# Optimization experiments

Hardware: AMD Instinct MI355X
Metric: run time of the kernel (lower is better)

Reference implementation:

```python
import jax, jax.numpy as jnp
import numpy as np

N_HEAD = 16

def setup_inputs() -> dict:
    key = jax.random.key(0)
    k1, k2 = jax.random.split(key)
    B, T, C = 4, 2048, 1024
    x = jax.random.normal(k1, (B, T, C), dtype=jnp.float32)
    # fused QKV projection weight, stored as [C, 3C] so qkv = x @ w_qkv
    # (equivalent to torch Linear(C, 3C, bias=False) with weight.T)
    w_qkv = jax.random.normal(k2, (C, 3 * C), dtype=jnp.float32) * (1.0 / np.sqrt(C))
    return {"x": x, "w_qkv": w_qkv}

def reference(x, w_qkv):
    B, T, C = x.shape
    H = N_HEAD
    D = C // H
    qkv = x @ w_qkv                                  # [B, T, 3C]
    q, k, v = jnp.split(qkv, 3, axis=2)              # each [B, T, C]
    q = q.reshape(B, T, H, D).transpose(0, 2, 1, 3)  # [B, H, T, D]
    k = k.reshape(B, T, H, D).transpose(0, 2, 1, 3)
    v = v.reshape(B, T, H, D).transpose(0, 2, 1, 3)
    scale = np.float32(1.0 / np.sqrt(D))
    att = jnp.einsum('bhqd,bhkd->bhqk', q, k) * scale   # [B, H, T, T]
    causal = jnp.tril(jnp.ones((T, T), dtype=bool))     # lower-tri = visible
    att = jnp.where(causal, att, -jnp.inf)
    att = jax.nn.softmax(att, axis=-1)
    out = jnp.einsum('bhqk,bhkd->bhqd', att, v)          # [B, H, T, D]
    return out.transpose(0, 2, 1, 3).reshape(B, T, C)
```

## Files before the change

kernel.cpp:

```cpp
#include <hip/hip_runtime.h>


#define B_ 4
#define T_ 2048
#define C_ 1024
#define H_ 16
#define D_ 64
#define QKV1 (B_*H_*T_*D_)

typedef __attribute__((ext_vector_type(4)))  float  f32x4;
typedef __attribute__((ext_vector_type(16))) float  f32x16;
typedef __attribute__((ext_vector_type(8)))  short  bf16x8;
typedef __attribute__((ext_vector_type(4)))  unsigned int u32x4;

__device__ inline unsigned short f2bf(float f) {
  unsigned int u = __builtin_bit_cast(unsigned int, f);
  u += 0x7FFFu + ((u >> 16) & 1u);
  return (unsigned short)(u >> 16);
}

__device__ inline void gload16(const unsigned short* g, unsigned short* l) {
  __builtin_amdgcn_global_load_lds(
      (const __attribute__((address_space(1))) void*)g,
      (__attribute__((address_space(3))) void*)l, 16, 0, 0);
}

__global__ __launch_bounds__(256) void convert_x(const float* __restrict__ x,
                                                 unsigned short* __restrict__ xb) {
  size_t i = ((size_t)blockIdx.x * 256 + threadIdx.x) * 16;
  f32x4 a = *(const f32x4*)(x + i);
  f32x4 b = *(const f32x4*)(x + i + 4);
  f32x4 c = *(const f32x4*)(x + i + 8);
  f32x4 d = *(const f32x4*)(x + i + 12);
  bf16x8 o0, o1;
#pragma unroll
  for (int j = 0; j < 4; j++) {
    o0[j]     = (short)f2bf(a[j]);
    o0[j + 4] = (short)f2bf(b[j]);
    o1[j]     = (short)f2bf(c[j]);
    o1[j + 4] = (short)f2bf(d[j]);
  }
  *(bf16x8*)(xb + i) = o0;
  *(bf16x8*)(xb + i + 8) = o1;
}

__global__ __launch_bounds__(256) void transpose_w(const float* __restrict__ w,
                                                   unsigned short* __restrict__ wt) {
  __shared__ float tile[32][33];
  const int tx = threadIdx.x & 31, ty = threadIdx.x >> 5;
  const int n0 = blockIdx.x * 32, k0 = blockIdx.y * 32;
#pragma unroll
  for (int j = 0; j < 4; j++) {
    int k = ty + j * 8;
    tile[k][tx] = w[(size_t)(k0 + k) * 3072 + n0 + tx];
  }
  __syncthreads();
#pragma unroll
  for (int j = 0; j < 4; j++) {
    int n = ty + j * 8;
    wt[(size_t)(n0 + n) * 1024 + k0 + tx] = f2bf(tile[tx][n]);
  }
}

__global__ __launch_bounds__(256) void qkv_gemm(const unsigned short* __restrict__ xb,
                                                const unsigned short* __restrict__ wt,
                                                unsigned short* __restrict__ qkv) {
  __shared__ unsigned short Al[128 * 64];
  __shared__ unsigned short Bl[128 * 64];
  const int tid = threadIdx.x;
  const int lane = tid & 63, wid = tid >> 6;
  const int l15 = lane & 15, g = lane >> 4;
  const int m0 = blockIdx.y * 128, n0 = blockIdx.x * 128;
  const int wm = (wid >> 1) * 64, wn = (wid & 1) * 64;

  f32x4 acc[4][4] = {};

  const int srow[4] = { (0 * 256 + tid) >> 3, (1 * 256 + tid) >> 3,
                        (2 * 256 + tid) >> 3, (3 * 256 + tid) >> 3 };
  int scol[4];
#pragma unroll
  for (int sw = 0; sw < 4; sw++) {
    int s = sw * 256 + tid;
    scol[sw] = (s & 7) ^ (srow[sw] & 7);
  }

  for (int k0 = 0; k0 < 1024; k0 += 64) {
    __syncthreads();
#pragma unroll
    for (int sw = 0; sw < 4; sw++) {
      unsigned short* ldsA = &Al[(sw * 256 + wid * 64) * 8];
      unsigned short* ldsB = &Bl[(sw * 256 + wid * 64) * 8];
      gload16(xb + (size_t)(m0 + srow[sw]) * 1024 + k0 + scol[sw] * 8, ldsA);
      gload16(wt + (size_t)(n0 + srow[sw]) * 1024 + k0 + scol[sw] * 8, ldsB);
    }
    __syncthreads();

#pragma unroll
    for (int ks = 0; ks < 2; ks++) {
      bf16x8 af[4], bfr[4];
#pragma unroll
      for (int mt = 0; mt < 4; mt++) {
        int row = wm + mt * 16 + l15;
        int c = (ks * 4 + g) ^ (row & 7);
        af[mt] = *(const bf16x8*)&Al[(row * 8 + c) * 8];
      }
#pragma unroll
      for (int nt = 0; nt < 4; nt++) {
        int row = wn + nt * 16 + l15;
        int c = (ks * 4 + g) ^ (row & 7);
        bfr[nt] = *(const bf16x8*)&Bl[(row * 8 + c) * 8];
      }
#pragma unroll
      for (int mt = 0; mt < 4; mt++)
#pragma unroll
        for (int nt = 0; nt < 4; nt++)
          acc[mt][nt] = __builtin_amdgcn_mfma_f32_16x16x32_bf16(af[mt], bfr[nt], acc[mt][nt], 0, 0, 0);
    }
  }

  const int r0 = g * 4, cc = l15;
#pragma unroll
  for (int mt = 0; mt < 4; mt++)
#pragma unroll
    for (int nt = 0; nt < 4; nt++)
#pragma unroll
      for (int r = 0; r < 4; r++) {
        int m = m0 + wm + mt * 16 + r0 + r;
        int n = n0 + wn + nt * 16 + cc;
        int b = m >> 11, t = m & 2047;
        int which = n >> 10, c = n & 1023;
        int h = c >> 6, d = c & 63;
        qkv[(size_t)which * QKV1 + ((size_t)((b * H_ + h) * T_ + t)) * D_ + d] =
            f2bf(acc[mt][nt][r]);
      }
}

__global__ __launch_bounds__(256) void attn(const unsigned short* __restrict__ qkv,
                                            float* __restrict__ out) {
  __shared__ unsigned short Kl[64][72];
  __shared__ unsigned short Vl[64][72];
  __shared__ float RSl[4][32];
  const int tid = threadIdx.x, lane = tid & 63, wq = tid >> 6;
  const int l31 = lane & 31, hi = lane >> 5;
  const int bh = blockIdx.y, xp = blockIdx.x;
  const int qta = xp, qtb = 31 - xp;
  const int ntiles = qtb + 1;
  const int member = wq >> 1;
  const int half = wq & 1;
  const int qt = member ? qta : qtb;
  const int q0 = qt * 64 + half * 32;
  const size_t base = (size_t)bh * (T_ * D_);
  const unsigned short* qp = qkv + base;
  const unsigned short* kp = qkv + (size_t)QKV1 + base;
  const unsigned short* vp = qkv + 2 * (size_t)QKV1 + base;

  bf16x8 qf[4];
#pragma unroll
  for (int c = 0; c < 4; c++) {
    bf16x8 v = *(const bf16x8*)(qp + (size_t)(q0 + l31) * 64 + c * 16 + hi * 8);
#pragma unroll
    for (int j = 0; j < 8; j++) {
      unsigned int u = (unsigned int)(unsigned short)v[j] << 16;
      float f = __builtin_bit_cast(float, u) * 0.125f;
      v[j] = (short)f2bf(f);
    }
    qf[c] = v;
  }

  f32x16 o0 = {}, o1 = {};
  float rs = 0.f;

  bf16x8 kreg0, kreg1, vreg0, vreg1;
  const int krow = tid >> 3, kch = tid & 7;
  const int vpr = tid >> 3, vdch = tid & 7;
#define LOADKV(IT)                                                             \
  do {                                                                         \
    size_t k0_ = (size_t)(IT) * 64;                                            \
    kreg0 = *(const bf16x8*)(kp + (k0_ + krow) * 64 + kch * 8);                \
    kreg1 = *(const bf16x8*)(kp + (k0_ + 32 + krow) * 64 + kch * 8);           \
    vreg0 = *(const bf16x8*)(vp + (k0_ + 2 * vpr) * 64 + vdch * 8);            \
    vreg1 = *(const bf16x8*)(vp + (k0_ + 2 * vpr + 1) * 64 + vdch * 8);        \
  } while (0)

  LOADKV(0);
  for (int it = 0; it < ntiles; ++it) {
    __syncthreads();
    *(bf16x8*)&Kl[krow][kch * 8] = kreg0;
    *(bf16x8*)&Kl[32 + krow][kch * 8] = kreg1;
#pragma unroll
    for (int j = 0; j < 8; j++) {
      int d = vdch * 8 + j;
      unsigned int pk = ((unsigned int)(unsigned short)vreg1[j] << 16) |
                        (unsigned int)(unsigned short)vreg0[j];
      *(unsigned int*)&Vl[d][(2 * vpr) ^ ((d >> 3) << 3)] = pk;
    }
    if (it + 1 < ntiles) LOADKV(it + 1);
    __syncthreads();

    if (it <= qt) {
      unsigned int pk_[16];
#pragma unroll
      for (int kt = 0; kt < 2; kt++) {
        f32x16 s = {};
        __builtin_amdgcn_s_setprio(1);
#pragma unroll
        for (int c = 0; c < 4; c++) {
          bf16x8 kf = *(const bf16x8*)&Kl[kt * 32 + l31][c * 16 + hi * 8];
          s = __builtin_amdgcn_mfma_f32_32x32x16_bf16(kf, qf[c], s, 0, 0, 0);
        }
        __builtin_amdgcn_s_setprio(0);
        if (it == qt) {
#pragma unroll
          for (int r = 0; r < 16; r++) {
            int kg = it * 64 + kt * 32 + (r & 3) + 8 * (r >> 2) + 4 * hi;
            if (kg > q0 + l31) s[r] = -1e30f;
          }
        }
        float p[16];
#pragma unroll
        for (int r = 0; r < 16; r++) { p[r] = __expf(s[r]); rs += p[r]; }
#pragma unroll
        for (int t = 0; t < 4; t++) {
          unsigned int plo, phi;
          asm("v_cvt_pk_bf16_f32 %0, %1, %2" : "=v"(plo) : "v"(p[4*t]), "v"(p[4*t+1]));
          asm("v_cvt_pk_bf16_f32 %0, %1, %2" : "=v"(phi) : "v"(p[4*t+2]), "v"(p[4*t+3]));
          pk_[(kt * 4 + t) * 2]     = plo;
          pk_[(kt * 4 + t) * 2 + 1] = phi;
        }
      }

      unsigned int rcv0[4], rcv1[4];
#pragma unroll
      for (int j = 0; j < 4; j++) {
        unsigned int s0 = hi ? pk_[(2 * j) * 2]     : pk_[(2 * j + 1) * 2];
        unsigned int s1 = hi ? pk_[(2 * j) * 2 + 1] : pk_[(2 * j + 1) * 2 + 1];
        rcv0[j] = (unsigned int)__shfl_xor((int)s0, 32);
        rcv1[j] = (unsigned int)__shfl_xor((int)s1, 32);
      }

      __builtin_amdgcn_s_setprio(1);
#pragma unroll
      for (int st = 0; st < 4; st++) {
        unsigned int u0 = hi ? rcv0[st]        : pk_[4 * st];
        unsigned int u1 = hi ? rcv1[st]        : pk_[4 * st + 1];
        unsigned int u2 = hi ? pk_[4 * st + 2] : rcv0[st];
        unsigned int u3 = hi ? pk_[4 * st + 3] : rcv1[st];
        u32x4 pu = {u0, u1, u2, u3};
        bf16x8 paf = __builtin_bit_cast(bf16x8, pu);
        int koff = st * 16 + hi * 8;
        bf16x8 vf0 = *(const bf16x8*)&Vl[l31][koff ^ ((l31 >> 3) << 3)];
        bf16x8 vf1 = *(const bf16x8*)&Vl[32 + l31][koff ^ (((32 + l31) >> 3) << 3)];
        o0 = __builtin_amdgcn_mfma_f32_32x32x16_bf16(paf, vf0, o0, 0, 0, 0);
        o1 = __builtin_amdgcn_mfma_f32_32x32x16_bf16(paf, vf1, o1, 0, 0, 0);
      }
      __builtin_amdgcn_s_setprio(0);
    }
  }

  float rsf = rs + __shfl_xor(rs, 32);
  float inv = 1.0f / rsf;
  if (hi == 0) RSl[wq][l31] = inv;
  asm volatile("s_waitcnt lgkmcnt(0)" ::: "memory");
  const int b = bh >> 4, h = bh & 15;
#pragma unroll
  for (int r = 0; r < 16; r++) {
    int ql = (r & 3) + 8 * (r >> 2) + 4 * hi;
    float iv = RSl[wq][ql];
    int qg = q0 + ql;
    size_t o = ((size_t)(b * T_ + qg)) * C_ + h * 64;
    out[o + l31]      = o0[r] * iv;
    out[o + 32 + l31] = o1[r] * iv;
  }
}

extern "C" void kernel_launch(void* const* d_in, const int* in_sizes, int n_in,
                              void* d_out, int out_size, void* d_ws, size_t ws_size,
                              hipStream_t stream) {
  const float* x = (const float*)d_in[0];
  const float* w = (const float*)d_in[1];
  float* out = (float*)d_out;
  unsigned short* wt  = (unsigned short*)d_ws;
  unsigned short* qkv = wt + (size_t)3072 * 1024;
  unsigned short* xb  = (unsigned short*)d_out;

  convert_x  <<<2048, 256, 0, stream>>>(x, xb);
  transpose_w<<<dim3(96, 32), 256, 0, stream>>>(w, wt);
  qkv_gemm   <<<dim3(24, 64), 256, 0, stream>>>(xb, wt, qkv);
  attn       <<<dim3(16, 64), 256, 0, stream>>>(qkv, out);
}
```

Measured before the change: 170.0 us.

## Split attention into one query tile per 128-thread block with rotated causal scheduling

The attention kernel no longer pairs a short and a long causal query tile in one 256-thread block. Each 128-thread block now processes a single 64-row query tile and loops only over the key tiles it needs, so waves no longer sit idle. A rotation across heads alternates ascending and descending tile order to balance load across the grid. Each thread now loads twice as many K/V vectors for LDS staging, and the 4-blocks-per-CU launch bound may constrain registers.

```diff
diff --git a/kernel.cpp b/kernel.cpp
--- a/kernel.cpp
+++ b/kernel.cpp
@@ -135,20 +135,19 @@
       }
 }
 
-__global__ __launch_bounds__(256) void attn(const unsigned short* __restrict__ qkv,
-                                            float* __restrict__ out) {
+__global__ __launch_bounds__(128, 4) void attn(const unsigned short* __restrict__ qkv,
+                                               float* __restrict__ out) {
   __shared__ unsigned short Kl[64][72];
   __shared__ unsigned short Vl[64][72];
-  __shared__ float RSl[4][32];
+  __shared__ float RSl[2][32];
   const int tid = threadIdx.x, lane = tid & 63, wq = tid >> 6;
   const int l31 = lane & 31, hi = lane >> 5;
-  const int bh = blockIdx.y, xp = blockIdx.x;
-  const int qta = xp, qtb = 31 - xp;
-  const int ntiles = qtb + 1;
-  const int member = wq >> 1;
-  const int half = wq & 1;
-  const int qt = member ? qta : qtb;
-  const int q0 = qt * 64 + half * 32;
+  const int bh = blockIdx.y;
+  const int jj = bh >> 3;
+  const int gg = (blockIdx.x + (jj >> 1) * 8) & 31;
+  const int qt = (jj & 1) ? (31 - gg) : gg;
+  const int ntiles = qt + 1;
+  const int q0 = qt * 64 + wq * 32;
   const size_t base = (size_t)bh * (T_ * D_);
   const unsigned short* qp = qkv + base;
   const unsigned short* kp = qkv + (size_t)QKV1 + base;
@@ -170,91 +169,98 @@
   f32x16 o0 = {}, o1 = {};
   float rs = 0.f;
 
-  bf16x8 kreg0, kreg1, vreg0, vreg1;
+  bf16x8 kreg0, kreg1, kreg2, kreg3, vr00, vr01, vr10, vr11;
   const int krow = tid >> 3, kch = tid & 7;
-  const int vpr = tid >> 3, vdch = tid & 7;
 #define LOADKV(IT)                                                             \
   do {                                                                         \
     size_t k0_ = (size_t)(IT) * 64;                                            \
-    kreg0 = *(const bf16x8*)(kp + (k0_ + krow) * 64 + kch * 8);                \
-    kreg1 = *(const bf16x8*)(kp + (k0_ + 32 + krow) * 64 + kch * 8);           \
-    vreg0 = *(const bf16x8*)(vp + (k0_ + 2 * vpr) * 64 + vdch * 8);            \
-    vreg1 = *(const bf16x8*)(vp + (k0_ + 2 * vpr + 1) * 64 + vdch * 8);        \
+    kreg0 = *(const bf16x8*)(kp + (k0_ + krow)      * 64 + kch * 8);           \
+    kreg1 = *(const bf16x8*)(kp + (k0_ + krow + 16) * 64 + kch * 8);           \
+    kreg2 = *(const bf16x8*)(kp + (k0_ + krow + 32) * 64 + kch * 8);           \
+    kreg3 = *(const bf16x8*)(kp + (k0_ + krow + 48) * 64 + kch * 8);           \
+    vr00  = *(const bf16x8*)(vp + (k0_ + 2 * krow)          * 64 + kch * 8);   \
+    vr01  = *(const bf16x8*)(vp + (k0_ + 2 * krow + 1)      * 64 + kch * 8);   \
+    vr10  = *(const bf16x8*)(vp + (k0_ + 2 * (krow + 16))     * 64 + kch * 8); \
+    vr11  = *(const bf16x8*)(vp + (k0_ + 2 * (krow + 16) + 1) * 64 + kch * 8); \
   } while (0)
 
   LOADKV(0);
   for (int it = 0; it < ntiles; ++it) {
     __syncthreads();
-    *(bf16x8*)&Kl[krow][kch * 8] = kreg0;
-    *(bf16x8*)&Kl[32 + krow][kch * 8] = kreg1;
+    *(bf16x8*)&Kl[krow][kch * 8]      = kreg0;
+    *(bf16x8*)&Kl[krow + 16][kch * 8] = kreg1;
+    *(bf16x8*)&Kl[krow + 32][kch * 8] = kreg2;
+    *(bf16x8*)&Kl[krow + 48][kch * 8] = kreg3;
 #pragma unroll
     for (int j = 0; j < 8; j++) {
-      int d = vdch * 8 + j;
-      unsigned int pk = ((unsigned int)(unsigned short)vreg1[j] << 16) |
-                        (unsigned int)(unsigned short)vreg0[j];
-      *(unsigned int*)&Vl[d][(2 * vpr) ^ ((d >> 3) << 3)] = pk;
+      int d = kch * 8 + j;
+      int sw = (d >> 3) << 3;
+      unsigned int pk0 = ((unsigned int)(unsigned short)vr01[j] << 16) |
+                         (unsigned int)(unsigned short)vr00[j];
+      unsigned int pk1 = ((unsigned int)(unsigned short)vr11[j] << 16) |
+                         (unsigned int)(unsigned short)vr10[j];
+      *(unsigned int*)&Vl[d][(2 * krow) ^ sw]        = pk0;
+      *(unsigned int*)&Vl[d][(2 * (krow + 16)) ^ sw] = pk1;
     }
     if (it + 1 < ntiles) LOADKV(it + 1);
     __syncthreads();
 
-    if (it <= qt) {
-      unsigned int pk_[16];
-#pragma unroll
-      for (int kt = 0; kt < 2; kt++) {
-        f32x16 s = {};
-        __builtin_amdgcn_s_setprio(1);
-#pragma unroll
-        for (int c = 0; c < 4; c++) {
-          bf16x8 kf = *(const bf16x8*)&Kl[kt * 32 + l31][c * 16 + hi * 8];
-          s = __builtin_amdgcn_mfma_f32_32x32x16_bf16(kf, qf[c], s, 0, 0, 0);
+    unsigned int pk_[16];
+#pragma unroll
+    for (int kt = 0; kt < 2; kt++) {
+      f32x16 s = {};
+      __builtin_amdgcn_s_setprio(1);
+#pragma unroll
+      for (int c = 0; c < 4; c++) {
+        bf16x8 kf = *(const bf16x8*)&Kl[kt * 32 + l31][c * 16 + hi * 8];
+        s = __builtin_amdgcn_mfma_f32_32x32x16_bf16(kf, qf[c], s, 0, 0, 0);
+      }
+      __builtin_amdgcn_s_setprio(0);
+      if (it == qt) {
+#pragma unroll
+        for (int r = 0; r < 16; r++) {
+          int kg = it * 64 + kt * 32 + (r & 3) + 8 * (r >> 2) + 4 * hi;
+          if (kg > q0 + l31) s[r] = -1e30f;
         }
-        __builtin_amdgcn_s_setprio(0);
-        if (it == qt) {
-#pragma unroll
-          for (int r = 0; r < 16; r++) {
-            int kg = it * 64 + kt * 32 + (r & 3) + 8 * (r >> 2) + 4 * hi;
-            if (kg > q0 + l31) s[r] = -1e30f;
-          }
-        }
-        float p[16];
-#pragma unroll
-        for (int r = 0; r < 16; r++) { p[r] = __expf(s[r]); rs += p[r]; }
-#pragma unroll
-        for (int t = 0; t < 4; t++) {
-          unsigned int plo, phi;
-          asm("v_cvt_pk_bf16_f32 %0, %1, %2" : "=v"(plo) : "v"(p[4*t]), "v"(p[4*t+1]));
-          asm("v_cvt_pk_bf16_f32 %0, %1, %2" : "=v"(phi) : "v"(p[4*t+2]), "v"(p[4*t+3]));
-          pk_[(kt * 4 + t) * 2]     = plo;
-          pk_[(kt * 4 + t) * 2 + 1] = phi;
-        }
-      }
-
-      unsigned int rcv0[4], rcv1[4];
-#pragma unroll
-      for (int j = 0; j < 4; j++) {
-        unsigned int s0 = hi ? pk_[(2 * j) * 2]     : pk_[(2 * j + 1) * 2];
-        unsigned int s1 = hi ? pk_[(2 * j) * 2 + 1] : pk_[(2 * j + 1) * 2 + 1];
-        rcv0[j] = (unsigned int)__shfl_xor((int)s0, 32);
-        rcv1[j] = (unsigned int)__shfl_xor((int)s1, 32);
-      }
-
-      __builtin_amdgcn_s_setprio(1);
-#pragma unroll
-      for (int st = 0; st < 4; st++) {
-        unsigned int u0 = hi ? rcv0[st]        : pk_[4 * st];
-        unsigned int u1 = hi ? rcv1[st]        : pk_[4 * st + 1];
-        unsigned int u2 = hi ? pk_[4 * st + 2] : rcv0[st];
-        unsigned int u3 = hi ? pk_[4 * st + 3] : rcv1[st];
-        u32x4 pu = {u0, u1, u2, u3};
-        bf16x8 paf = __builtin_bit_cast(bf16x8, pu);
-        int koff = st * 16 + hi * 8;
-        bf16x8 vf0 = *(const bf16x8*)&Vl[l31][koff ^ ((l31 >> 3) << 3)];
-        bf16x8 vf1 = *(const bf16x8*)&Vl[32 + l31][koff ^ (((32 + l31) >> 3) << 3)];
-        o0 = __builtin_amdgcn_mfma_f32_32x32x16_bf16(paf, vf0, o0, 0, 0, 0);
-        o1 = __builtin_amdgcn_mfma_f32_32x32x16_bf16(paf, vf1, o1, 0, 0, 0);
-      }
-      __builtin_amdgcn_s_setprio(0);
-    }
+      }
+      float p[16];
+#pragma unroll
+      for (int r = 0; r < 16; r++) { p[r] = __expf(s[r]); rs += p[r]; }
+#pragma unroll
+      for (int t = 0; t < 4; t++) {
+        unsigned int plo, phi;
+        asm("v_cvt_pk_bf16_f32 %0, %1, %2" : "=v"(plo) : "v"(p[4*t]), "v"(p[4*t+1]));
+        asm("v_cvt_pk_bf16_f32 %0, %1, %2" : "=v"(phi) : "v"(p[4*t+2]), "v"(p[4*t+3]));
+        pk_[(kt * 4 + t) * 2]     = plo;
+        pk_[(kt * 4 + t) * 2 + 1] = phi;
+      }
+    }
+
+    unsigned int rcv0[4], rcv1[4];
+#pragma unroll
+    for (int j = 0; j < 4; j++) {
+      unsigned int s0 = hi ? pk_[(2 * j) * 2]     : pk_[(2 * j + 1) * 2];
+      unsigned int s1 = hi ? pk_[(2 * j) * 2 + 1] : pk_[(2 * j + 1) * 2 + 1];
+      rcv0[j] = (unsigned int)__shfl_xor((int)s0, 32);
+      rcv1[j] = (unsigned int)__shfl_xor((int)s1, 32);
+    }
+
+    __builtin_amdgcn_s_setprio(1);
+#pragma unroll
+    for (int st = 0; st < 4; st++) {
+      unsigned int u0 = hi ? rcv0[st]        : pk_[4 * st];
+      unsigned int u1 = hi ? rcv1[st]        : pk_[4 * st + 1];
+      unsigned int u2 = hi ? pk_[4 * st + 2] : rcv0[st];
+      unsigned int u3 = hi ? pk_[4 * st + 3] : rcv1[st];
+      u32x4 pu = {u0, u1, u2, u3};
+      bf16x8 paf = __builtin_bit_cast(bf16x8, pu);
+      int koff = st * 16 + hi * 8;
+      bf16x8 vf0 = *(const bf16x8*)&Vl[l31][koff ^ ((l31 >> 3) << 3)];
+      bf16x8 vf1 = *(const bf16x8*)&Vl[32 + l31][koff ^ (((32 + l31) >> 3) << 3)];
+      o0 = __builtin_amdgcn_mfma_f32_32x32x16_bf16(paf, vf0, o0, 0, 0, 0);
+      o1 = __builtin_amdgcn_mfma_f32_32x32x16_bf16(paf, vf1, o1, 0, 0, 0);
+    }
+    __builtin_amdgcn_s_setprio(0);
   }
 
   float rsf = rs + __shfl_xor(rs, 32);
@@ -286,5 +292,5 @@
   convert_x  <<<2048, 256, 0, stream>>>(x, xb);
   transpose_w<<<dim3(96, 32), 256, 0, stream>>>(w, wt);
   qkv_gemm   <<<dim3(24, 64), 256, 0, stream>>>(xb, wt, qkv);
-  attn       <<<dim3(16, 64), 256, 0, stream>>>(qkv, out);
-}
+  attn       <<<dim3(32, 64), 128, 0, stream>>>(qkv, out);
+}
```

Result: slower. 221.8 us (+30.5%).
